# Kernel optimization log

Measured on AMD Instinct MI355X. Metric: run time of the kernel, lower is better.

Reference implementation:

```python
import jax, jax.numpy as jnp
import numpy as np

B, U, L, H = 2048, 512, 32, 64  # batch, num_units, latent_dim, hidden


def setup_inputs() -> dict:
    key = jax.random.key(0)
    ks = jax.random.split(key, 17)
    s = 0.05  # weight scale
    inp = {
        "x": jax.random.normal(ks[0], (B, U), dtype=jnp.float32),
        # encoder: U -> 64 -> 64 -> 64 -> L
        "We1": jax.random.normal(ks[1], (U, H), jnp.float32) * s,
        "be1": jnp.zeros((H,), jnp.float32),
        "We2": jax.random.normal(ks[2], (H, H), jnp.float32) * s,
        "be2": jnp.zeros((H,), jnp.float32),
        "We3": jax.random.normal(ks[3], (H, H), jnp.float32) * s,
        "be3": jnp.zeros((H,), jnp.float32),
        "We4": jax.random.normal(ks[4], (H, L), jnp.float32) * s,
        "be4": jnp.zeros((L,), jnp.float32),
        # U disjoint decoders, weights stacked along unit axis: L -> 64 -> 64 -> 64 -> 1
        "Wd1": jax.random.normal(ks[5], (U, L, H), jnp.float32) * s,
        "bd1": jnp.zeros((U, H), jnp.float32),
        "Wd2": jax.random.normal(ks[6], (U, H, H), jnp.float32) * s,
        "bd2": jnp.zeros((U, H), jnp.float32),
        "Wd3": jax.random.normal(ks[7], (U, H, H), jnp.float32) * s,
        "bd3": jnp.zeros((U, H), jnp.float32),
        "Wd4": jax.random.normal(ks[8], (U, H), jnp.float32) * s,  # last layer out_dim=1, squeezed
        "bd4": jnp.zeros((U,), jnp.float32),
    }
    return inp


def reference(x, We1, be1, We2, be2, We3, be3, We4, be4,
              Wd1, bd1, Wd2, bd2, Wd3, bd3, Wd4, bd4):
    # shared encoder MLP: [B, U] -> [B, L]
    z = jax.nn.relu(x @ We1 + be1)
    z = jax.nn.relu(z @ We2 + be2)
    z = jax.nn.relu(z @ We3 + be3)
    z = z @ We4 + be4  # [B, L]
    # all U decoders batched as grouped GEMMs: [B, L] -> [B, U]
    h = jax.nn.relu(jnp.einsum('bl,ulh->buh', z, Wd1) + bd1)   # [B, U, H]
    h = jax.nn.relu(jnp.einsum('buh,uhk->buk', h, Wd2) + bd2)  # [B, U, H]
    h = jax.nn.relu(jnp.einsum('buh,uhk->buk', h, Wd3) + bd3)  # [B, U, H]
    out = jnp.einsum('buh,uh->bu', h, Wd4) + bd4               # [B, U]
    return out
```

## Files before the change

kernel.cpp:

```cpp
#include <hip/hip_runtime.h>
#include <hip/hip_bf16.h>
#include <hip/hip_fp16.h>
#include <stdint.h>

#define NB 2048
#define NU 512
#define NL 32
#define NH 64

typedef float    f4    __attribute__((ext_vector_type(4)));
typedef uint32_t u32x4 __attribute__((ext_vector_type(4)));
typedef _Float16 h8    __attribute__((ext_vector_type(8)));
typedef _Float16 h2    __attribute__((ext_vector_type(2)));

__device__ __forceinline__ f4 mfma16h(u32x4 a, u32x4 b, f4 c) {
    return __builtin_amdgcn_mfma_f32_16x16x32_f16(
        __builtin_bit_cast(h8, a), __builtin_bit_cast(h8, b), c, 0, 0, 0);
}

__device__ __forceinline__ uint32_t pk2h(float a, float b) {
    uint32_t la = (uint32_t)__half_as_ushort(__float2half_rn(a));
    uint32_t hb = (uint32_t)__half_as_ushort(__float2half_rn(b));
    return la | (hb << 16);
}

__device__ __forceinline__ uint32_t pk_rtz(float e, float o) {
    return __builtin_bit_cast(uint32_t, __builtin_amdgcn_cvt_pkrtz(e, o));
}

__device__ __forceinline__ uint32_t pk_relu(float e, float o) {
    uint32_t r = pk_rtz(e, o);
    asm("v_pk_max_f16 %0, %1, 0" : "=v"(r) : "v"(r));
    return r;
}

__device__ __forceinline__ float dot2(uint32_t a, uint32_t b, float c) {
    return __builtin_amdgcn_fdot2(__builtin_bit_cast(h2, a),
                                  __builtin_bit_cast(h2, b), c, false);
}

__global__ __launch_bounds__(256)
void enc_kernel(const float* __restrict__ x,
                const float* __restrict__ We1, const float* __restrict__ be1,
                const float* __restrict__ We2, const float* __restrict__ be2,
                const float* __restrict__ We3, const float* __restrict__ be3,
                const float* __restrict__ We4, const float* __restrict__ be4,
                uint32_t* __restrict__ zpk)
{
    const int RE = 8;
    __shared__ float xs[RE][512];
    __shared__ float ws[128 * 64];
    __shared__ float h[RE][NH];
    __shared__ float h2s[RE][NH];

    const int t  = threadIdx.x;
    const int r0 = blockIdx.x * RE;

    {
        const f4* xv  = (const f4*)(x + (size_t)r0 * 512);
        f4*       xsv = (f4*)&xs[0][0];
        for (int i = t; i < RE * 512 / 4; i += 256) xsv[i] = xv[i];
    }

    const int j = t & 63;
    const int w = t >> 6;

    float acc0 = be1[j], acc1 = be1[j];
    for (int kc = 0; kc < 512; kc += 128) {
        __syncthreads();
        const f4* wv  = (const f4*)(We1 + (size_t)kc * 64);
        f4*       wsv = (f4*)ws;
        for (int i = t; i < 128 * 64 / 4; i += 256) wsv[i] = wv[i];
        __syncthreads();
        #pragma unroll 8
        for (int k = 0; k < 128; ++k) {
            float wval = ws[k * 64 + j];
            acc0 = fmaf(xs[w][kc + k],     wval, acc0);
            acc1 = fmaf(xs[w + 4][kc + k], wval, acc1);
        }
    }
    acc0 = fmaxf(acc0, 0.f); acc1 = fmaxf(acc1, 0.f);
    __syncthreads();
    h[w][j] = acc0; h[w + 4][j] = acc1;
    __syncthreads();

    acc0 = be2[j]; acc1 = be2[j];
    #pragma unroll
    for (int k = 0; k < 64; ++k) {
        float wval = We2[k * 64 + j];
        acc0 = fmaf(h[w][k],     wval, acc0);
        acc1 = fmaf(h[w + 4][k], wval, acc1);
    }
    acc0 = fmaxf(acc0, 0.f); acc1 = fmaxf(acc1, 0.f);
    h2s[w][j] = acc0; h2s[w + 4][j] = acc1;
    __syncthreads();

    acc0 = be3[j]; acc1 = be3[j];
    #pragma unroll
    for (int k = 0; k < 64; ++k) {
        float wval = We3[k * 64 + j];
        acc0 = fmaf(h2s[w][k],     wval, acc0);
        acc1 = fmaf(h2s[w + 4][k], wval, acc1);
    }
    acc0 = fmaxf(acc0, 0.f); acc1 = fmaxf(acc1, 0.f);
    h[w][j] = acc0; h[w + 4][j] = acc1;
    __syncthreads();

    const int j4  = t & 31;
    const int row = t >> 5;
    float acc = be4[j4];
    #pragma unroll
    for (int k = 0; k < 64; ++k)
        acc = fmaf(h[row][k], We4[k * 32 + j4], acc);
    float nb = __shfl_xor(acc, 1);
    if ((j4 & 1) == 0)
        zpk[(size_t)(r0 + row) * 16 + (j4 >> 1)] = pk2h(acc, nb);
}

template <int K2>
__device__ __forceinline__ void stageW(const float* __restrict__ g,
                                       uint32_t (*dst)[68], int t)
{
    for (int g4 = t; g4 < K2 * 16; g4 += 256) {
        const int k2 = g4 >> 4, c4 = (g4 & 15) << 2;
        f4 a = *(const f4*)(g + (size_t)(2 * k2) * NH + c4);
        f4 b = *(const f4*)(g + (size_t)(2 * k2 + 1) * NH + c4);
        u32x4 p;
        p[0] = pk2h(a[0], b[0]);
        p[1] = pk2h(a[1], b[1]);
        p[2] = pk2h(a[2], b[2]);
        p[3] = pk2h(a[3], b[3]);
        *(u32x4*)&dst[k2][c4] = p;
    }
}

__global__ __launch_bounds__(256)
void dec_kernel(const uint32_t* __restrict__ zpk,
                const float* __restrict__ Wd1, const float* __restrict__ bd1,
                const float* __restrict__ Wd2, const float* __restrict__ bd2,
                const float* __restrict__ Wd3, const float* __restrict__ bd3,
                const float* __restrict__ Wd4, const float* __restrict__ bd4,
                float* __restrict__ out)
{
    __shared__ uint32_t wpk1[16][68];
    __shared__ uint32_t wpk2[32][68];
    __shared__ uint32_t wpk3[150][68];
    __shared__ float bsh[3][NH];
    __shared__ float w4s[NH];

    const int bid = blockIdx.x;
    const int u = ((bid & 7) << 4) | (((bid >> 3) & 3) << 7) | (bid >> 5);
    const int t = threadIdx.x;

    stageW<16>(Wd1 + (size_t)u * NL * NH, wpk1, t);
    stageW<32>(Wd2 + (size_t)u * NH * NH, wpk2, t);
    stageW<32>(Wd3 + (size_t)u * NH * NH, wpk3, t);
    if (t < NH) {
        bsh[0][t] = bd1[(size_t)u * NH + t];
        bsh[1][t] = bd2[(size_t)u * NH + t];
        bsh[2][t] = bd3[(size_t)u * NH + t];
        w4s[t]    = Wd4[(size_t)u * NH + t];
    }
    __syncthreads();

    const int w  = t >> 6;
    const int lr = t & 15;
    const int lg = (t & 63) >> 4;
    const float b4 = bd4[u];

    int cperm[4];
    #pragma unroll
    for (int mt = 0; mt < 4; ++mt)
        cperm[mt] = ((mt >> 1) << 5) + ((lr >> 2) << 3) + ((mt & 1) << 2) + (lr & 3);

    u32x4 a1[4], a2[4][2], a3[4][2];
    #pragma unroll
    for (int mt = 0; mt < 4; ++mt) {
        const int c = cperm[mt];
        #pragma unroll
        for (int i = 0; i < 4; ++i)
            a1[mt][i] = wpk1[lg * 4 + i][c];
        #pragma unroll
        for (int ks = 0; ks < 2; ++ks) {
            #pragma unroll
            for (int i = 0; i < 4; ++i) {
                a2[mt][ks][i] = wpk2[ks * 16 + lg * 4 + i][c];
                a3[mt][ks][i] = wpk3[ks * 16 + lg * 4 + i][c];
            }
        }
    }

    int bq[4];
    #pragma unroll
    for (int mt = 0; mt < 4; ++mt)
        bq[mt] = ((mt >> 1) << 5) + (lg << 3) + ((mt & 1) << 2);

    f4 bc1[4], bc2[4], bc3[4];
    #pragma unroll
    for (int mt = 0; mt < 4; ++mt) {
        bc1[mt] = *(const f4*)&bsh[0][bq[mt]];
        bc2[mt] = *(const f4*)&bsh[1][bq[mt]];
        bc3[mt] = *(const f4*)&bsh[2][bq[mt]];
    }

    uint32_t wd4pk[4][2];
    #pragma unroll
    for (int mt = 0; mt < 4; ++mt) {
        wd4pk[mt][0] = pk2h(w4s[bq[mt]],     w4s[bq[mt] + 1]);
        wd4pk[mt][1] = pk2h(w4s[bq[mt] + 2], w4s[bq[mt] + 3]);
    }

    const int rl = w * 16 + lr;

    u32x4 zc[2];
    zc[0] = *(const u32x4*)(zpk + (size_t)rl * 16 + lg * 4);
    zc[1] = *(const u32x4*)(zpk + (size_t)(64 + rl) * 16 + lg * 4);

    for (int it = 0; it < 16; ++it) {
        const int rb  = it * 128 + rl;
        const int rbn = ((it + 1) & 15) * 128 + rl;
        u32x4 zn[2];
        zn[0] = *(const u32x4*)(zpk + (size_t)rbn * 16 + lg * 4);
        zn[1] = *(const u32x4*)(zpk + (size_t)(rbn + 64) * 16 + lg * 4);

        f4 acc[2][4];

        #pragma unroll
        for (int s = 0; s < 2; ++s)
            #pragma unroll
            for (int mt = 0; mt < 4; ++mt)
                acc[s][mt] = mfma16h(a1[mt], zc[s], bc1[mt]);

        u32x4 bf0[2], bf1[2];
        #pragma unroll
        for (int s = 0; s < 2; ++s) {
            bf0[s][0] = pk_relu(acc[s][0][0], acc[s][0][1]);
            bf0[s][1] = pk_relu(acc[s][0][2], acc[s][0][3]);
            bf0[s][2] = pk_relu(acc[s][1][0], acc[s][1][1]);
            bf0[s][3] = pk_relu(acc[s][1][2], acc[s][1][3]);
            bf1[s][0] = pk_relu(acc[s][2][0], acc[s][2][1]);
            bf1[s][1] = pk_relu(acc[s][2][2], acc[s][2][3]);
            bf1[s][2] = pk_relu(acc[s][3][0], acc[s][3][1]);
            bf1[s][3] = pk_relu(acc[s][3][2], acc[s][3][3]);
        }

        #pragma unroll
        for (int s = 0; s < 2; ++s)
            #pragma unroll
            for (int mt = 0; mt < 4; ++mt)
                acc[s][mt] = mfma16h(a2[mt][0], bf0[s], bc2[mt]);
        #pragma unroll
        for (int s = 0; s < 2; ++s)
            #pragma unroll
            for (int mt = 0; mt < 4; ++mt)
                acc[s][mt] = mfma16h(a2[mt][1], bf1[s], acc[s][mt]);

        #pragma unroll
        for (int s = 0; s < 2; ++s) {
            bf0[s][0] = pk_relu(acc[s][0][0], acc[s][0][1]);
            bf0[s][1] = pk_relu(acc[s][0][2], acc[s][0][3]);
            bf0[s][2] = pk_relu(acc[s][1][0], acc[s][1][1]);
            bf0[s][3] = pk_relu(acc[s][1][2], acc[s][1][3]);
            bf1[s][0] = pk_relu(acc[s][2][0], acc[s][2][1]);
            bf1[s][1] = pk_relu(acc[s][2][2], acc[s][2][3]);
            bf1[s][2] = pk_relu(acc[s][3][0], acc[s][3][1]);
            bf1[s][3] = pk_relu(acc[s][3][2], acc[s][3][3]);
        }

        #pragma unroll
        for (int s = 0; s < 2; ++s)
            #pragma unroll
            for (int mt = 0; mt < 4; ++mt)
                acc[s][mt] = mfma16h(a3[mt][0], bf0[s], bc3[mt]);
        #pragma unroll
        for (int s = 0; s < 2; ++s)
            #pragma unroll
            for (int mt = 0; mt < 4; ++mt)
                acc[s][mt] = mfma16h(a3[mt][1], bf1[s], acc[s][mt]);

        #pragma unroll
        for (int s = 0; s < 2; ++s) {
            float pa = 0.f, pb = 0.f;
            #pragma unroll
            for (int mt = 0; mt < 4; ++mt) {
                uint32_t p0 = pk_relu(acc[s][mt][0], acc[s][mt][1]);
                uint32_t p1 = pk_relu(acc[s][mt][2], acc[s][mt][3]);
                pa = dot2(p0, wd4pk[mt][0], pa);
                pb = dot2(p1, wd4pk[mt][1], pb);
            }
            float part = pa + pb;
            part += __shfl_xor(part, 16);
            part += __shfl_xor(part, 32);
            if ((t & 48) == 0)
                out[(size_t)(rb + s * 64) * NU + u] = part + b4;
        }

        zc[0] = zn[0]; zc[1] = zn[1];
    }
}

extern "C" void kernel_launch(void* const* d_in, const int* in_sizes, int n_in,
                              void* d_out, int out_size, void* d_ws, size_t ws_size,
                              hipStream_t stream)
{
    const float* x   = (const float*)d_in[0];
    const float* We1 = (const float*)d_in[1];
    const float* be1 = (const float*)d_in[2];
    const float* We2 = (const float*)d_in[3];
    const float* be2 = (const float*)d_in[4];
    const float* We3 = (const float*)d_in[5];
    const float* be3 = (const float*)d_in[6];
    const float* We4 = (const float*)d_in[7];
    const float* be4 = (const float*)d_in[8];
    const float* Wd1 = (const float*)d_in[9];
    const float* bd1 = (const float*)d_in[10];
    const float* Wd2 = (const float*)d_in[11];
    const float* bd2 = (const float*)d_in[12];
    const float* Wd3 = (const float*)d_in[13];
    const float* bd3 = (const float*)d_in[14];
    const float* Wd4 = (const float*)d_in[15];
    const float* bd4 = (const float*)d_in[16];
    float* out = (float*)d_out;

    uint32_t* zpk = (uint32_t*)d_ws;

    enc_kernel<<<NB / 8, 256, 0, stream>>>(x, We1, be1, We2, be2, We3, be3,
                                           We4, be4, zpk);
    dec_kernel<<<NU, 256, 0, stream>>>(zpk, Wd1, bd1, Wd2, bd2,
                                       Wd3, bd3, Wd4, bd4, out);
}
```

Baseline: 48.30 us.

## Split decoder batch across two blocks per unit and widen encoder blocks

The decoder grid doubles so that each unit's batch of 2048 rows is split into two halves. Each block handles 8 iterations instead of 16, which gives 1024 blocks for the MI355X's CUs instead of 512. The encoder now uses 512 threads with one row per thread instead of two, and the padded LDS array wpk3 shrinks from 150 to 72 rows. In exchange, decoder weights are staged and converted to fp16 twice per unit, and encoder work per thread is lower while the final layer leaves half the threads idle.

```diff
diff --git a/kernel.cpp b/kernel.cpp
--- a/kernel.cpp
+++ b/kernel.cpp
@@ -39,7 +39,7 @@
                                   __builtin_bit_cast(h2, b), c, false);
 }
 
-__global__ __launch_bounds__(256)
+__global__ __launch_bounds__(512)
 void enc_kernel(const float* __restrict__ x,
                 const float* __restrict__ We1, const float* __restrict__ be1,
                 const float* __restrict__ We2, const float* __restrict__ be2,
@@ -59,62 +59,55 @@
     {
         const f4* xv  = (const f4*)(x + (size_t)r0 * 512);
         f4*       xsv = (f4*)&xs[0][0];
-        for (int i = t; i < RE * 512 / 4; i += 256) xsv[i] = xv[i];
+        for (int i = t; i < RE * 512 / 4; i += 512) xsv[i] = xv[i];
     }
 
     const int j = t & 63;
     const int w = t >> 6;
 
-    float acc0 = be1[j], acc1 = be1[j];
+    float acc0 = be1[j];
     for (int kc = 0; kc < 512; kc += 128) {
         __syncthreads();
         const f4* wv  = (const f4*)(We1 + (size_t)kc * 64);
         f4*       wsv = (f4*)ws;
-        for (int i = t; i < 128 * 64 / 4; i += 256) wsv[i] = wv[i];
+        for (int i = t; i < 128 * 64 / 4; i += 512) wsv[i] = wv[i];
         __syncthreads();
         #pragma unroll 8
-        for (int k = 0; k < 128; ++k) {
-            float wval = ws[k * 64 + j];
-            acc0 = fmaf(xs[w][kc + k],     wval, acc0);
-            acc1 = fmaf(xs[w + 4][kc + k], wval, acc1);
-        }
-    }
-    acc0 = fmaxf(acc0, 0.f); acc1 = fmaxf(acc1, 0.f);
-    __syncthreads();
-    h[w][j] = acc0; h[w + 4][j] = acc1;
-    __syncthreads();
-
-    acc0 = be2[j]; acc1 = be2[j];
-    #pragma unroll
-    for (int k = 0; k < 64; ++k) {
-        float wval = We2[k * 64 + j];
-        acc0 = fmaf(h[w][k],     wval, acc0);
-        acc1 = fmaf(h[w + 4][k], wval, acc1);
-    }
-    acc0 = fmaxf(acc0, 0.f); acc1 = fmaxf(acc1, 0.f);
-    h2s[w][j] = acc0; h2s[w + 4][j] = acc1;
-    __syncthreads();
-
-    acc0 = be3[j]; acc1 = be3[j];
-    #pragma unroll
-    for (int k = 0; k < 64; ++k) {
-        float wval = We3[k * 64 + j];
-        acc0 = fmaf(h2s[w][k],     wval, acc0);
-        acc1 = fmaf(h2s[w + 4][k], wval, acc1);
-    }
-    acc0 = fmaxf(acc0, 0.f); acc1 = fmaxf(acc1, 0.f);
-    h[w][j] = acc0; h[w + 4][j] = acc1;
-    __syncthreads();
-
-    const int j4  = t & 31;
-    const int row = t >> 5;
-    float acc = be4[j4];
+        for (int k = 0; k < 128; ++k)
+            acc0 = fmaf(xs[w][kc + k], ws[k * 64 + j], acc0);
+    }
+    acc0 = fmaxf(acc0, 0.f);
+    __syncthreads();
+    h[w][j] = acc0;
+    __syncthreads();
+
+    acc0 = be2[j];
     #pragma unroll
     for (int k = 0; k < 64; ++k)
-        acc = fmaf(h[row][k], We4[k * 32 + j4], acc);
-    float nb = __shfl_xor(acc, 1);
-    if ((j4 & 1) == 0)
-        zpk[(size_t)(r0 + row) * 16 + (j4 >> 1)] = pk2h(acc, nb);
+        acc0 = fmaf(h[w][k], We2[k * 64 + j], acc0);
+    acc0 = fmaxf(acc0, 0.f);
+    h2s[w][j] = acc0;
+    __syncthreads();
+
+    acc0 = be3[j];
+    #pragma unroll
+    for (int k = 0; k < 64; ++k)
+        acc0 = fmaf(h2s[w][k], We3[k * 64 + j], acc0);
+    acc0 = fmaxf(acc0, 0.f);
+    h[w][j] = acc0;
+    __syncthreads();
+
+    if (t < 256) {
+        const int j4  = t & 31;
+        const int row = t >> 5;
+        float acc = be4[j4];
+        #pragma unroll
+        for (int k = 0; k < 64; ++k)
+            acc = fmaf(h[row][k], We4[k * 32 + j4], acc);
+        float nb = __shfl_xor(acc, 1);
+        if ((j4 & 1) == 0)
+            zpk[(size_t)(r0 + row) * 16 + (j4 >> 1)] = pk2h(acc, nb);
+    }
 }
 
 template <int K2>
@@ -144,12 +137,14 @@
 {
     __shared__ uint32_t wpk1[16][68];
     __shared__ uint32_t wpk2[32][68];
-    __shared__ uint32_t wpk3[150][68];
+    __shared__ uint32_t wpk3[72][68];
     __shared__ float bsh[3][NH];
     __shared__ float w4s[NH];
 
-    const int bid = blockIdx.x;
-    const int u = ((bid & 7) << 4) | (((bid >> 3) & 3) << 7) | (bid >> 5);
+    const int bid  = blockIdx.x;
+    const int half = bid >> 9;
+    const int ub   = bid & 511;
+    const int u = ((ub & 7) << 4) | (((ub >> 3) & 3) << 7) | (ub >> 5);
     const int t = threadIdx.x;
 
     stageW<16>(Wd1 + (size_t)u * NL * NH, wpk1, t);
@@ -210,15 +205,16 @@
         wd4pk[mt][1] = pk2h(w4s[bq[mt] + 2], w4s[bq[mt] + 3]);
     }
 
-    const int rl = w * 16 + lr;
+    const int rl  = w * 16 + lr;
+    const int it0 = half * 8;
 
     u32x4 zc[2];
-    zc[0] = *(const u32x4*)(zpk + (size_t)rl * 16 + lg * 4);
-    zc[1] = *(const u32x4*)(zpk + (size_t)(64 + rl) * 16 + lg * 4);
-
-    for (int it = 0; it < 16; ++it) {
+    zc[0] = *(const u32x4*)(zpk + (size_t)(it0 * 128 + rl) * 16 + lg * 4);
+    zc[1] = *(const u32x4*)(zpk + (size_t)(it0 * 128 + 64 + rl) * 16 + lg * 4);
+
+    for (int it = it0; it < it0 + 8; ++it) {
         const int rb  = it * 128 + rl;
-        const int rbn = ((it + 1) & 15) * 128 + rl;
+        const int rbn = (it0 + ((it - it0 + 1) & 7)) * 128 + rl;
         u32x4 zn[2];
         zn[0] = *(const u32x4*)(zpk + (size_t)rbn * 16 + lg * 4);
         zn[1] = *(const u32x4*)(zpk + (size_t)(rbn + 64) * 16 + lg * 4);
@@ -324,8 +320,8 @@
 
     uint32_t* zpk = (uint32_t*)d_ws;
 
-    enc_kernel<<<NB / 8, 256, 0, stream>>>(x, We1, be1, We2, be2, We3, be3,
+    enc_kernel<<<NB / 8, 512, 0, stream>>>(x, We1, be1, We2, be2, We3, be3,
                                            We4, be4, zpk);
-    dec_kernel<<<NU, 256, 0, stream>>>(zpk, Wd1, bd1, Wd2, bd2,
-                                       Wd3, bd3, Wd4, bd4, out);
-}
+    dec_kernel<<<NU * 2, 256, 0, stream>>>(zpk, Wd1, bd1, Wd2, bd2,
+                                           Wd3, bd3, Wd4, bd4, out);
+}
```

New measurement: 47.65 us. No clear change (-1.4%).
